# Optimization experiments

Hardware: AMD Instinct MI355X
Metric: run time of the kernel (lower is better)

The kernel has to match this reference:

```python
import jax, jax.numpy as jnp
import numpy as np

B, T, CIN, HID, OUT, H, W = 8, 8, 128, 64, 64, 32, 32


def _conv(x, w, b):
    # x: [B, C, H, W], w: [O, C, kh, kw] -> SAME-padded conv, stride 1
    y = jax.lax.conv_general_dilated(x, w, (1, 1), "SAME",
                                     dimension_numbers=("NCHW", "OIHW", "NCHW"))
    return y + b[None, :, None, None]


def _layer_dir(xs, w_ih, w_hh, b_ih, b_hh, reverse):
    # xs: [T, B, C, H, W]; one direction of a ConvLSTM layer; returns hs [T, B, HID, H, W]
    b, hh_, ww_ = xs.shape[1], xs.shape[3], xs.shape[4]
    h0 = jnp.zeros((b, HID, hh_, ww_), xs.dtype)

    def step(carry, x):
        h, c = carry
        gates = _conv(x, w_ih, b_ih) + _conv(h, w_hh, b_hh)  # [B, 4*HID, H, W]
        i, f, g, o = jnp.split(gates, 4, axis=1)
        c = jax.nn.sigmoid(f) * c + jax.nn.sigmoid(i) * jnp.tanh(g)
        h = jax.nn.sigmoid(o) * jnp.tanh(c)
        return (h, c), h

    _, hs = jax.lax.scan(step, (h0, h0), xs, reverse=reverse)
    return hs


def _forward(features, w_ih0f, w_hh0f, b_ih0f, b_hh0f,
             w_ih0r, w_hh0r, b_ih0r, b_hh0r,
             w_ih1f, w_hh1f, b_ih1f, b_hh1f,
             w_ih1r, w_hh1r, b_ih1r, b_hh1r,
             w_out, b_out):
    xs = jnp.transpose(features, (1, 0, 2, 3, 4))  # [T, B, C, H, W]
    # layer 0, both directions (scan reverse=True aligns outputs to original time order)
    hf = _layer_dir(xs, w_ih0f, w_hh0f, b_ih0f, b_hh0f, False)
    hr = _layer_dir(xs, w_ih0r, w_hh0r, b_ih0r, b_hh0r, True)
    xs1 = jnp.concatenate([hf, hr], axis=2)  # [T, B, 2*HID, H, W] (dropout is identity at eval)
    # layer 1
    hf1 = _layer_dir(xs1, w_ih1f, w_hh1f, b_ih1f, b_hh1f, False)
    hr1 = _layer_dir(xs1, w_ih1r, w_hh1r, b_ih1r, b_hh1r, True)
    last = jnp.concatenate([hf1[-1], hr1[-1]], axis=1)  # output[:, -1] -> [B, 2*HID, H, W]
    return jax.nn.relu(_conv(last, w_out, b_out))


def setup_inputs() -> dict:
    key = jax.random.key(0)
    ks = jax.random.split(key, 24)
    G = 4 * HID
    p = lambda k, s: jax.random.normal(k, s, jnp.float32) * 0.05
    d = {"features": jax.random.normal(ks[0], (B, T, CIN, H, W), jnp.float32)}
    i = 1
    for l, cin in ((0, CIN), (1, 2 * HID)):
        for dr in ("f", "r"):
            d[f"w_ih{l}{dr}"] = p(ks[i], (G, cin, 3, 3)); i += 1
            d[f"w_hh{l}{dr}"] = p(ks[i], (G, HID, 3, 3)); i += 1
            d[f"b_ih{l}{dr}"] = p(ks[i], (G,)); i += 1
            d[f"b_hh{l}{dr}"] = p(ks[i], (G,)); i += 1
    d["w_out"] = p(ks[i], (OUT, 2 * HID, 1, 1)); i += 1
    d["b_out"] = p(ks[i], (OUT,))
    return d


def reference(features, w_ih0f, w_hh0f, b_ih0f, b_hh0f,
              w_ih0r, w_hh0r, b_ih0r, b_hh0r,
              w_ih1f, w_hh1f, b_ih1f, b_hh1f,
              w_ih1r, w_hh1r, b_ih1r, b_hh1r,
              w_out, b_out):
    return _forward(features, w_ih0f, w_hh0f, b_ih0f, b_hh0f,
                    w_ih0r, w_hh0r, b_ih0r, b_hh0r,
                    w_ih1f, w_hh1f, b_ih1f, b_hh1f,
                    w_ih1r, w_hh1r, b_ih1r, b_hh1r,
                    w_out, b_out)
```

## Files before the change

### kernel.cpp

```cpp
#include <hip/hip_runtime.h>
#include <math.h>
#include <stdint.h>


typedef __attribute__((ext_vector_type(8))) short short8;
typedef __attribute__((ext_vector_type(4))) float float4v;

namespace {
constexpr int IMG = 34 * 34 * 64;
constexpr size_t SLOTI = 16ull * IMG;
constexpr int ROWB = 34 * 128;
constexpr int PADB = 8192;
}
template <int N> struct IC { static constexpr int v = N; };

__device__ __forceinline__ uint16_t bf16_rne(float x) {
  uint32_t u = __builtin_bit_cast(uint32_t, x);
  return (uint16_t)((u + 0x7FFFu + ((u >> 16) & 1u)) >> 16);
}
__device__ __forceinline__ float bf16_to_f(uint16_t h) {
  uint32_t u = ((uint32_t)h) << 16;
  return __builtin_bit_cast(float, u);
}

__device__ __forceinline__ void gl_lds16(const void* g, void* l) {
  __builtin_amdgcn_global_load_lds(
      (const __attribute__((address_space(1))) void*)g,
      (__attribute__((address_space(3))) void*)l, 16, 0, 0);
}

__global__ void pack_features(const float* __restrict__ f, uint16_t* __restrict__ out) {
  const size_t i = (size_t)blockIdx.x * 256 + threadIdx.x;
  const int blk_s = (int)(i & 7);
  size_t pp = i >> 3;
  const int px = (int)(pp % 34); pp /= 34;
  const int yy = (int)(pp % 34); pp /= 34;
  const int cg = (int)(pp & 3);
  const int bt = (int)(pp >> 2);
  const int b = bt & 7, t = bt >> 3;
  const int blk = blk_s ^ (px & 7);
  const int pl = blk >> 2, kg = blk & 3;
  short8 sv;
  if (px == 0 || px == 33 || yy == 0 || yy == 33) {
    #pragma unroll
    for (int j = 0; j < 8; ++j) sv[j] = 0;
  } else {
    const int x = px - 1, y = yy - 1;
    #pragma unroll
    for (int j = 0; j < 8; ++j) {
      const int ch = cg * 32 + kg * 8 + j;
      const float fv = f[(((size_t)b * 8 + t) * 128 + ch) * 1024 + y * 32 + x];
      const uint16_t hi = bf16_rne(fv);
      sv[j] = (short)(pl ? bf16_rne(fv - bf16_to_f(hi)) : hi);
    }
  }
  *(short8*)(out + i * 8) = sv;
}

struct WPackArgs {
  const float* wih[4]; const float* whh[4];
  const float* bih[4]; const float* bhh[4];
  uint32_t* wp; float* bp;
};
__global__ void pack_weights(WPackArgs A) {
  const int combo = blockIdx.y;
  const int idx = blockIdx.x * 256 + threadIdx.x;
  const int q = idx & 4095;
  const int rest = idx >> 12;
  const int nt = rest & 1;
  const int ct = rest >> 1;
  const int tap = ct % 9, cg = ct / 9;
  const int w2 = q & 3;
  const int b8s = (q >> 2) & 7;
  const int hcp = (q >> 5) & 15;
  const int g = (q >> 9) & 3;
  const int pl = (q >> 11) & 1;
  const int b8 = b8s ^ (hcp & 7);
  const int kg = b8 & 3;
  const int hcl = hcp * 2 + (b8 >> 2);
  const int n = g * 64 + nt * 32 + hcl;
  const float* wih = A.wih[combo];
  const float* whh = A.whh[combo];
  uint32_t out = 0;
  #pragma unroll
  for (int e = 0; e < 2; ++e) {
    const int ch = cg * 32 + kg * 8 + w2 * 2 + e;
    const float wv = (ch < 128) ? wih[((size_t)n * 128 + ch) * 9 + tap]
                                : whh[((size_t)n * 64 + (ch - 128)) * 9 + tap];
    const uint16_t hi = bf16_rne(wv);
    const uint16_t v = pl ? bf16_rne(wv - bf16_to_f(hi)) : hi;
    out |= ((uint32_t)v) << (16 * e);
  }
  A.wp[(size_t)combo * 442368 + idx] = out;
  if (idx < 256) A.bp[combo * 256 + idx] = A.bih[combo][idx] + A.bhh[combo][idx];
}

struct StepArgs {
  const uint16_t* in0; const uint16_t* in1; const uint16_t* in2;
  int nc0, nc1, nc2;
  const uint32_t* W;
  const float* bias;
  float* cbuf;
  uint16_t* himg;
  float* hf32;
};

struct Frags { short8 a[2][2]; short8 w[2][4]; };

__global__ __launch_bounds__(512, 2) void conv_lstm_step(StepArgs A0, StepArgs A1) {
  extern __shared__ char smem[];
  char* Asm_ = smem;
  char* Wsm_ = smem + 65536;

  const StepArgs a = (blockIdx.z == 0) ? A0 : A1;
  const int bx = blockIdx.x;
  const int nt = bx & 1;
  const int band = (bx >> 1) & 7;
  const int b = bx >> 4;
  const int y0 = band * 4;
  const int tid = threadIdx.x;
  const int lane = tid & 63;
  const int w = tid >> 6;
  const int m15 = lane & 15;
  const int kg = lane >> 4;
  const int r = w & 3;
  const int hcg = w >> 2;

  int offA[2][3][2];
  #pragma unroll
  for (int xh = 0; xh < 2; ++xh)
    #pragma unroll
    for (int kx = 0; kx < 3; ++kx)
      #pragma unroll
      for (int pl = 0; pl < 2; ++pl) {
        const int px = xh * 16 + kx + m15;
        const int sw = (pl * 4 + kg) ^ (px & 7);
        offA[xh][kx][pl] = r * ROWB + px * 128 + sw * 16;
      }
  int offW[2][4];
  {
    const int hcp = hcg * 8 + (m15 >> 1);
    const int b8 = kg + 4 * (m15 & 1);
    #pragma unroll
    for (int pl = 0; pl < 2; ++pl)
      #pragma unroll
      for (int g = 0; g < 4; ++g)
        offW[pl][g] = (((pl * 4 + g) * 16 + hcp) * 8 + (b8 ^ (hcp & 7))) * 16;
  }

  const int ncg = a.nc0 + a.nc1 + a.nc2;
  auto abase = [&](int cg) -> const char* {
    const uint16_t* t;
    if (cg < a.nc0) t = a.in0 + ((size_t)b * a.nc0 + cg) * IMG;
    else if (cg < a.nc0 + a.nc1) t = a.in1 + ((size_t)b * a.nc1 + (cg - a.nc0)) * IMG;
    else t = a.in2 + ((size_t)b * a.nc2 + (cg - a.nc0 - a.nc1)) * IMG;
    return (const char*)t + (size_t)y0 * ROWB;
  };
  auto stageA = [&](int cgi, int par) {
    const char* g = abase(cgi);
    char* d = Asm_ + par * 32768;
    #pragma unroll
    for (int j = 0; j < 4; ++j)
      gl_lds16(g + (size_t)(4 * w + j) * 1024 + lane * 16, d + (4 * w + j) * 1024);
  };
  auto stageW = [&](int cgs, int taps, int slot) {
    const char* g = (const char*)a.W + ((size_t)((cgs * 9 + taps) * 2 + nt) << 14);
    char* d = Wsm_ + slot * 16384;
    #pragma unroll
    for (int j = 0; j < 2; ++j)
      gl_lds16(g + (size_t)(2 * w + j) * 1024 + lane * 16, d + (2 * w + j) * 1024);
  };
  auto read_frags = [&](auto tapc, int cgn, int lin1) -> Frags {
    constexpr int TN = decltype(tapc)::v;
    constexpr int ky = TN / 3, kx = TN % 3;
    Frags f;
    const char* Ab = Asm_ + (cgn & 1) * 32768 + ky * ROWB;
    const char* Wb = Wsm_ + (lin1 & 3) * 16384;
    #pragma unroll
    for (int xh = 0; xh < 2; ++xh)
      #pragma unroll
      for (int pl = 0; pl < 2; ++pl)
        f.a[xh][pl] = *(const short8*)(Ab + offA[xh][kx][pl]);
    #pragma unroll
    for (int pl = 0; pl < 2; ++pl)
      #pragma unroll
      for (int g = 0; g < 4; ++g)
        f.w[pl][g] = *(const short8*)(Wb + offW[pl][g]);
    return f;
  };

  float4v acc[2][4];
  #pragma unroll
  for (int xh = 0; xh < 2; ++xh)
    #pragma unroll
    for (int g = 0; g < 4; ++g) acc[xh][g] = (float4v){0.f, 0.f, 0.f, 0.f};

  stageA(0, 0);
  stageW(0, 0, 0);
  stageW(0, 1, 1);
  stageW(0, 2, 2);
  asm volatile("s_waitcnt vmcnt(2)\n\ts_barrier" ::: "memory");
  Frags cur = read_frags(IC<0>{}, 0, 0);

  for (int cg = 0; cg < ncg; ++cg) {
    auto tap_body = [&](auto tapc) {
      constexpr int TAP = decltype(tapc)::v;
      constexpr int CNT = (TAP == 1 || TAP == 2) ? 6 : 2;
      asm volatile("s_waitcnt vmcnt(%0)\n\ts_barrier" :: "n"(CNT) : "memory");
      const int lin = cg * 9 + TAP;
      {
        const int l3 = lin + 3;
        int cgs = l3 / 9;
        const int taps = l3 % 9;
        if (cgs >= ncg) cgs = 0;
        stageW(cgs, taps, l3 & 3);
      }
      if (TAP == 0) {
        const int nx = (cg + 1 < ncg) ? cg + 1 : 0;
        stageA(nx, (cg + 1) & 1);
      }
      constexpr int TN = (TAP + 1) % 9;
      Frags nxt = read_frags(IC<TN>{}, cg + (TAP == 8 ? 1 : 0), lin + 1);
      #pragma unroll
      for (int xh = 0; xh < 2; ++xh)
        #pragma unroll
        for (int g = 0; g < 4; ++g) {
          acc[xh][g] = __builtin_amdgcn_mfma_f32_16x16x32_bf16(cur.a[xh][0], cur.w[0][g], acc[xh][g], 0, 0, 0);
          acc[xh][g] = __builtin_amdgcn_mfma_f32_16x16x32_bf16(cur.a[xh][0], cur.w[1][g], acc[xh][g], 0, 0, 0);
          acc[xh][g] = __builtin_amdgcn_mfma_f32_16x16x32_bf16(cur.a[xh][1], cur.w[0][g], acc[xh][g], 0, 0, 0);
        }
      cur = nxt;
    };
    tap_body(IC<0>{}); tap_body(IC<1>{}); tap_body(IC<2>{});
    tap_body(IC<3>{}); tap_body(IC<4>{}); tap_body(IC<5>{});
    tap_body(IC<6>{}); tap_body(IC<7>{}); tap_body(IC<8>{});
  }
  asm volatile("s_waitcnt vmcnt(0)" ::: "memory");

  const int hcl = hcg * 16 + m15;
  const int hc = nt * 32 + hcl;
  const int y = y0 + r;
  float bi[4];
  #pragma unroll
  for (int g = 0; g < 4; ++g) bi[g] = a.bias[g * 64 + hc];
  float* crow = a.cbuf + ((size_t)(b * 64 + hc)) * 1024 + y * 32;
  float* hrow = a.hf32 ? a.hf32 + ((size_t)(b * 64 + hc)) * 1024 + y * 32 : nullptr;
  uint16_t* hb = a.himg ? a.himg + ((size_t)(b * 2 + nt)) * IMG : nullptr;
  const int kgb = hcl >> 3, jj = hcl & 7;
  #pragma unroll
  for (int xh = 0; xh < 2; ++xh) {
    const int x0 = xh * 16 + kg * 4;
    float4v cv = *(float4v*)(crow + x0);
    float4v cn, hn;
    #pragma unroll
    for (int q = 0; q < 4; ++q) {
      const float ig = 1.f / (1.f + expf(-(acc[xh][0][q] + bi[0])));
      const float fg = 1.f / (1.f + expf(-(acc[xh][1][q] + bi[1])));
      const float gg = tanhf(acc[xh][2][q] + bi[2]);
      const float og = 1.f / (1.f + expf(-(acc[xh][3][q] + bi[3])));
      const float c2 = fg * cv[q] + ig * gg;
      cn[q] = c2;
      hn[q] = og * tanhf(c2);
    }
    *(float4v*)(crow + x0) = cn;
    if (hrow) *(float4v*)(hrow + x0) = hn;
    if (hb) {
      #pragma unroll
      for (int q = 0; q < 4; ++q) {
        const int px = x0 + q + 1;
        const int sw = px & 7;
        const uint16_t hi = bf16_rne(hn[q]);
        const uint16_t lo = bf16_rne(hn[q] - bf16_to_f(hi));
        const size_t p16 = ((size_t)(y + 1) * 34 + px) * 64;
        hb[p16 + (size_t)(kgb ^ sw) * 8 + jj] = hi;
        hb[p16 + (size_t)((4 + kgb) ^ sw) * 8 + jj] = lo;
      }
    }
  }
  if (hb) {
    {
      const int rr = tid >> 7;
      const int hlf = (tid >> 6) & 1;
      const int jx = tid & 63;
      hb[((size_t)(y0 + 1 + rr) * 34 + hlf * 33) * 64 + jx] = 0;
    }
    if (band == 0) for (int i = tid; i < 2176; i += 512) hb[i] = 0;
    if (band == 7) for (int i = tid; i < 2176; i += 512) hb[(size_t)33 * 2176 + i] = 0;
  }
}

__global__ void final_conv(const float* __restrict__ h1f_last, const float* __restrict__ h1r_last,
                           const float* __restrict__ wout, const float* __restrict__ bout,
                           float* __restrict__ out) {
  __shared__ float Ws[16 * 128];
  const int oq = blockIdx.y;
  for (int i = threadIdx.x; i < 16 * 128; i += 256) Ws[i] = wout[oq * 16 * 128 + i];
  __syncthreads();
  const int gp = blockIdx.x * 256 + threadIdx.x;
  const int b = gp >> 10, p = gp & 1023;
  float acc[16];
  #pragma unroll
  for (int o = 0; o < 16; ++o) acc[o] = bout[oq * 16 + o];
  for (int c = 0; c < 128; ++c) {
    const float xv = (c < 64) ? h1f_last[((size_t)b * 64 + c) * 1024 + p]
                              : h1r_last[((size_t)b * 64 + (c - 64)) * 1024 + p];
    #pragma unroll
    for (int o = 0; o < 16; ++o) acc[o] = fmaf(xv, Ws[o * 128 + c], acc[o]);
  }
  #pragma unroll
  for (int o = 0; o < 16; ++o) {
    const float v = acc[o];
    out[((size_t)b * 64 + oq * 16 + o) * 1024 + p] = v > 0.f ? v : 0.f;
  }
}

extern "C" void kernel_launch(void* const* d_in, const int* in_sizes, int n_in,
                              void* d_out, int out_size, void* d_ws, size_t ws_size,
                              hipStream_t stream) {
  char* p = (char*)d_ws;
  uint16_t* featImg = (uint16_t*)p; p += (size_t)8 * 8 * 4 * IMG * 2 + PADB;
  uint32_t* WP = (uint32_t*)p;      p += (size_t)4 * 442368 * 4;
  float* bp = (float*)p;            p += 4096;
  uint16_t* hf0i = (uint16_t*)p;    p += (size_t)9 * SLOTI * 2 + PADB;
  uint16_t* hr0i = (uint16_t*)p;    p += (size_t)9 * SLOTI * 2 + PADB;
  uint16_t* h1fi = (uint16_t*)p;    p += (size_t)2 * SLOTI * 2 + PADB;
  float* c0f = (float*)p;           p += (size_t)4 * 2097152;
  float* c0r = c0f + 524288;
  float* c1f = c0r + 524288;
  float* c1r = c1f + 524288;
  float* h1f8 = (float*)p;          p += 2097152;
  float* h1r8 = (float*)p;          p += 2097152;

  hipMemsetAsync(c0f, 0, (size_t)4 * 2097152, stream);
  hipMemsetAsync(hf0i, 0, (size_t)SLOTI * 2, stream);
  hipMemsetAsync(hr0i + (size_t)8 * SLOTI, 0, (size_t)SLOTI * 2, stream);
  hipMemsetAsync(h1fi, 0, (size_t)SLOTI * 2, stream);

  pack_features<<<dim3(9248), 256, 0, stream>>>((const float*)d_in[0], featImg);

  WPackArgs wa;
  for (int combo = 0; combo < 4; ++combo) {
    const int base = 1 + combo * 4;
    wa.wih[combo] = (const float*)d_in[base];
    wa.whh[combo] = (const float*)d_in[base + 1];
    wa.bih[combo] = (const float*)d_in[base + 2];
    wa.bhh[combo] = (const float*)d_in[base + 3];
  }
  wa.wp = WP; wa.bp = bp;
  pack_weights<<<dim3(1728, 4), 256, 0, stream>>>(wa);

  constexpr int DYN_LDS = 131072;
  (void)hipFuncSetAttribute((const void*)conv_lstm_step,
                            hipFuncAttributeMaxDynamicSharedMemorySize, DYN_LDS);

  auto mk = [&](const uint16_t* i0, int n0, const uint16_t* i1, int n1,
                const uint16_t* i2, int n2, int combo, float* cb,
                uint16_t* himg, float* hf32) {
    StepArgs s;
    s.in0 = i0; s.in1 = i1; s.in2 = i2;
    s.nc0 = n0; s.nc1 = n1; s.nc2 = n2;
    s.W = WP + (size_t)combo * 442368; s.bias = bp + combo * 256;
    s.cbuf = cb; s.himg = himg; s.hf32 = hf32;
    return s;
  };

  for (int k = 0; k < 8; ++k) {
    const int tr = 7 - k;
    StepArgs f = mk(featImg + (size_t)k * 8 * 4 * IMG, 4,
                    hf0i + (size_t)k * SLOTI, 2, nullptr, 0,
                    0, c0f, hf0i + (size_t)(k + 1) * SLOTI, nullptr);
    StepArgs r = mk(featImg + (size_t)tr * 8 * 4 * IMG, 4,
                    hr0i + (size_t)(tr + 1) * SLOTI, 2, nullptr, 0,
                    1, c0r, hr0i + (size_t)tr * SLOTI, nullptr);
    conv_lstm_step<<<dim3(128, 1, 2), 512, DYN_LDS, stream>>>(f, r);
  }

  for (int t = 0; t < 8; ++t) {
    uint16_t* himg = (t < 7) ? h1fi + (size_t)((t + 1) & 1) * SLOTI : nullptr;
    float* hf32 = (t == 7) ? h1f8 : nullptr;
    StepArgs s = mk(hf0i + (size_t)(t + 1) * SLOTI, 2, hr0i + (size_t)t * SLOTI, 2,
                    h1fi + (size_t)(t & 1) * SLOTI, 2, 2, c1f, himg, hf32);
    if (t == 0) {
      StepArgs rv = mk(hf0i + (size_t)8 * SLOTI, 2, hr0i + (size_t)7 * SLOTI, 2,
                       nullptr, 0, 3, c1r, nullptr, h1r8);
      conv_lstm_step<<<dim3(128, 1, 2), 512, DYN_LDS, stream>>>(s, rv);
    } else {
      conv_lstm_step<<<dim3(128, 1, 1), 512, DYN_LDS, stream>>>(s, s);
    }
  }

  final_conv<<<dim3(32, 4), 256, 0, stream>>>(
      h1f8, h1r8, (const float*)d_in[17], (const float*)d_in[18], (float*)d_out);
}
```

Measured before the change: 773.9 us.

## Halve workgroup size, raise per-wave M tile, add band-size templated launches

The ConvLSTM step kernel now runs 4 waves per workgroup instead of 8. Each wave owns multiple rows of M fragments (MROWS/2 rows x 2 halves), so each weight fragment read from LDS feeds more MFMAs. The kernel is templated on rows per band: layer 0 keeps 4-row bands with 128 blocks, and layer 1 uses 2-row bands with 256 blocks to fill more CUs in the sequential steps. It also double-buffers fragments explicitly with asm register pinning and changes the staging chunk counts and waitcnt thresholds to match. The risks are higher register pressure, lower occupancy (launch bounds 256,1) and fragile vmcnt accounting.

After: 750.0 us. 1.03x faster.

```diff
diff --git a/kernel.cpp b/kernel.cpp
--- a/kernel.cpp
+++ b/kernel.cpp
@@ -27,6 +27,22 @@
   __builtin_amdgcn_global_load_lds(
       (const __attribute__((address_space(1))) void*)g,
       (__attribute__((address_space(3))) void*)l, 16, 0, 0);
+}
+
+template <int NMF> struct Frags { short8 a[NMF][2]; short8 w[2][4]; };
+
+__device__ __forceinline__ void pin_frags(Frags<4>& f) {
+  asm volatile("" : "+v"(f.a[0][0]), "+v"(f.a[0][1]), "+v"(f.a[1][0]), "+v"(f.a[1][1]),
+                    "+v"(f.a[2][0]), "+v"(f.a[2][1]), "+v"(f.a[3][0]), "+v"(f.a[3][1]),
+                    "+v"(f.w[0][0]), "+v"(f.w[0][1]), "+v"(f.w[0][2]), "+v"(f.w[0][3]),
+                    "+v"(f.w[1][0]), "+v"(f.w[1][1]), "+v"(f.w[1][2]), "+v"(f.w[1][3])
+               :: "memory");
+}
+__device__ __forceinline__ void pin_frags(Frags<2>& f) {
+  asm volatile("" : "+v"(f.a[0][0]), "+v"(f.a[0][1]), "+v"(f.a[1][0]), "+v"(f.a[1][1]),
+                    "+v"(f.w[0][0]), "+v"(f.w[0][1]), "+v"(f.w[0][2]), "+v"(f.w[0][3]),
+                    "+v"(f.w[1][0]), "+v"(f.w[1][1]), "+v"(f.w[1][2]), "+v"(f.w[1][3])
+               :: "memory");
 }
 
 __global__ void pack_features(const float* __restrict__ f, uint16_t* __restrict__ out) {
@@ -105,9 +121,12 @@
   float* hf32;
 };
 
-struct Frags { short8 a[2][2]; short8 w[2][4]; };
-
-__global__ __launch_bounds__(512, 2) void conv_lstm_step(StepArgs A0, StepArgs A1) {
+template <int MROWS>
+__global__ __launch_bounds__(256, 1) void conv_lstm_step(StepArgs A0, StepArgs A1) {
+  constexpr int R = MROWS / 2;
+  constexpr int NMF = MROWS;
+  constexpr int ACH = (MROWS == 4) ? 7 : 5;
+  constexpr int NBANDS = 32 / MROWS;
   extern __shared__ char smem[];
   char* Asm_ = smem;
   char* Wsm_ = smem + 65536;
@@ -115,18 +134,18 @@
   const StepArgs a = (blockIdx.z == 0) ? A0 : A1;
   const int bx = blockIdx.x;
   const int nt = bx & 1;
-  const int band = (bx >> 1) & 7;
-  const int b = bx >> 4;
-  const int y0 = band * 4;
+  const int band = (bx >> 1) & (NBANDS - 1);
+  const int b = bx >> ((MROWS == 4) ? 4 : 5);
+  const int y0 = band * MROWS;
   const int tid = threadIdx.x;
   const int lane = tid & 63;
   const int w = tid >> 6;
   const int m15 = lane & 15;
   const int kg = lane >> 4;
-  const int r = w & 3;
-  const int hcg = w >> 2;
-
-  int offA[2][3][2];
+  const int hcg = w & 1;
+  const int mh = w >> 1;
+
+  int offA0[2][3][2];
   #pragma unroll
   for (int xh = 0; xh < 2; ++xh)
     #pragma unroll
@@ -135,7 +154,7 @@
       for (int pl = 0; pl < 2; ++pl) {
         const int px = xh * 16 + kx + m15;
         const int sw = (pl * 4 + kg) ^ (px & 7);
-        offA[xh][kx][pl] = r * ROWB + px * 128 + sw * 16;
+        offA0[xh][kx][pl] = px * 128 + sw * 16;
       }
   int offW[2][4];
   {
@@ -147,6 +166,7 @@
       for (int g = 0; g < 4; ++g)
         offW[pl][g] = (((pl * 4 + g) * 16 + hcp) * 8 + (b8 ^ (hcp & 7))) * 16;
   }
+  const int mrow = mh * R * ROWB;
 
   const int ncg = a.nc0 + a.nc1 + a.nc2;
   auto abase = [&](int cg) -> const char* {
@@ -160,132 +180,157 @@
     const char* g = abase(cgi);
     char* d = Asm_ + par * 32768;
     #pragma unroll
-    for (int j = 0; j < 4; ++j)
-      gl_lds16(g + (size_t)(4 * w + j) * 1024 + lane * 16, d + (4 * w + j) * 1024);
+    for (int j = 0; j < ACH; ++j)
+      gl_lds16(g + (size_t)(ACH * w + j) * 1024 + lane * 16, d + (ACH * w + j) * 1024);
   };
   auto stageW = [&](int cgs, int taps, int slot) {
     const char* g = (const char*)a.W + ((size_t)((cgs * 9 + taps) * 2 + nt) << 14);
     char* d = Wsm_ + slot * 16384;
     #pragma unroll
-    for (int j = 0; j < 2; ++j)
-      gl_lds16(g + (size_t)(2 * w + j) * 1024 + lane * 16, d + (2 * w + j) * 1024);
-  };
-  auto read_frags = [&](auto tapc, int cgn, int lin1) -> Frags {
-    constexpr int TN = decltype(tapc)::v;
+    for (int j = 0; j < 4; ++j)
+      gl_lds16(g + (size_t)(4 * w + j) * 1024 + lane * 16, d + (4 * w + j) * 1024);
+  };
+
+  Frags<NMF> f0, f1;
+  auto read_frags = [&](auto tnc, int par, int wslot, Frags<NMF>& f) {
+    constexpr int TN = decltype(tnc)::v;
     constexpr int ky = TN / 3, kx = TN % 3;
-    Frags f;
-    const char* Ab = Asm_ + (cgn & 1) * 32768 + ky * ROWB;
-    const char* Wb = Wsm_ + (lin1 & 3) * 16384;
-    #pragma unroll
-    for (int xh = 0; xh < 2; ++xh)
-      #pragma unroll
-      for (int pl = 0; pl < 2; ++pl)
-        f.a[xh][pl] = *(const short8*)(Ab + offA[xh][kx][pl]);
+    const char* Ab = Asm_ + par * 32768 + mrow;
+    const char* Wb = Wsm_ + wslot * 16384;
+    #pragma unroll
+    for (int rr = 0; rr < R; ++rr)
+      #pragma unroll
+      for (int xh = 0; xh < 2; ++xh)
+        #pragma unroll
+        for (int pl = 0; pl < 2; ++pl)
+          f.a[rr * 2 + xh][pl] = *(const short8*)(Ab + (rr + ky) * ROWB + offA0[xh][kx][pl]);
     #pragma unroll
     for (int pl = 0; pl < 2; ++pl)
       #pragma unroll
       for (int g = 0; g < 4; ++g)
         f.w[pl][g] = *(const short8*)(Wb + offW[pl][g]);
-    return f;
-  };
-
-  float4v acc[2][4];
-  #pragma unroll
-  for (int xh = 0; xh < 2; ++xh)
-    #pragma unroll
-    for (int g = 0; g < 4; ++g) acc[xh][g] = (float4v){0.f, 0.f, 0.f, 0.f};
+  };
+
+  float4v acc[NMF][4];
+  #pragma unroll
+  for (int mf = 0; mf < NMF; ++mf)
+    #pragma unroll
+    for (int g = 0; g < 4; ++g) acc[mf][g] = (float4v){0.f, 0.f, 0.f, 0.f};
+
+  auto do_mfma = [&](Frags<NMF>& f) {
+    #pragma unroll
+    for (int mf = 0; mf < NMF; ++mf)
+      #pragma unroll
+      for (int g = 0; g < 4; ++g) {
+        acc[mf][g] = __builtin_amdgcn_mfma_f32_16x16x32_bf16(f.a[mf][0], f.w[0][g], acc[mf][g], 0, 0, 0);
+        acc[mf][g] = __builtin_amdgcn_mfma_f32_16x16x32_bf16(f.a[mf][0], f.w[1][g], acc[mf][g], 0, 0, 0);
+        acc[mf][g] = __builtin_amdgcn_mfma_f32_16x16x32_bf16(f.a[mf][1], f.w[0][g], acc[mf][g], 0, 0, 0);
+      }
+  };
+
+  auto window = [&](auto tapc, auto parc, int cg, int lin9) {
+    constexpr int TAP = decltype(tapc)::v;
+    constexpr int P = decltype(parc)::v;
+    constexpr int CNT = (TAP == 1 || TAP == 2) ? 4 + ACH : 4;
+    asm volatile("s_waitcnt vmcnt(%0)\n\ts_barrier" :: "n"(CNT) : "memory");
+    {
+      const int l3 = lin9 + TAP + 3;
+      int cgs = l3 / 9;
+      const int taps = l3 % 9;
+      if (cgs >= ncg) cgs = 0;
+      stageW(cgs, taps, l3 & 3);
+    }
+    if (TAP == 0) {
+      const int nx = (cg + 1 < ncg) ? cg + 1 : 0;
+      stageA(nx, (cg + 1) & 1);
+    }
+    constexpr int TN = (TAP + 1) % 9;
+    const int cgn = cg + (TAP == 8 ? 1 : 0);
+    read_frags(IC<TN>{}, cgn & 1, (lin9 + TAP + 1) & 3, P ? f0 : f1);
+    Frags<NMF>& cur = P ? f1 : f0;
+    pin_frags(cur);
+    do_mfma(cur);
+  };
+  auto run9 = [&](auto cgpc, int cg) {
+    constexpr int CGP = decltype(cgpc)::v;
+    const int lin9 = cg * 9;
+    window(IC<0>{}, IC<(CGP + 0) & 1>{}, cg, lin9);
+    window(IC<1>{}, IC<(CGP + 1) & 1>{}, cg, lin9);
+    window(IC<2>{}, IC<(CGP + 2) & 1>{}, cg, lin9);
+    window(IC<3>{}, IC<(CGP + 3) & 1>{}, cg, lin9);
+    window(IC<4>{}, IC<(CGP + 4) & 1>{}, cg, lin9);
+    window(IC<5>{}, IC<(CGP + 5) & 1>{}, cg, lin9);
+    window(IC<6>{}, IC<(CGP + 6) & 1>{}, cg, lin9);
+    window(IC<7>{}, IC<(CGP + 7) & 1>{}, cg, lin9);
+    window(IC<8>{}, IC<(CGP + 8) & 1>{}, cg, lin9);
+  };
 
   stageA(0, 0);
   stageW(0, 0, 0);
   stageW(0, 1, 1);
   stageW(0, 2, 2);
-  asm volatile("s_waitcnt vmcnt(2)\n\ts_barrier" ::: "memory");
-  Frags cur = read_frags(IC<0>{}, 0, 0);
+  asm volatile("s_waitcnt vmcnt(8)\n\ts_barrier" ::: "memory");
+  read_frags(IC<0>{}, 0, 0, f0);
 
   for (int cg = 0; cg < ncg; ++cg) {
-    auto tap_body = [&](auto tapc) {
-      constexpr int TAP = decltype(tapc)::v;
-      constexpr int CNT = (TAP == 1 || TAP == 2) ? 6 : 2;
-      asm volatile("s_waitcnt vmcnt(%0)\n\ts_barrier" :: "n"(CNT) : "memory");
-      const int lin = cg * 9 + TAP;
-      {
-        const int l3 = lin + 3;
-        int cgs = l3 / 9;
-        const int taps = l3 % 9;
-        if (cgs >= ncg) cgs = 0;
-        stageW(cgs, taps, l3 & 3);
-      }
-      if (TAP == 0) {
-        const int nx = (cg + 1 < ncg) ? cg + 1 : 0;
-        stageA(nx, (cg + 1) & 1);
-      }
-      constexpr int TN = (TAP + 1) % 9;
-      Frags nxt = read_frags(IC<TN>{}, cg + (TAP == 8 ? 1 : 0), lin + 1);
-      #pragma unroll
-      for (int xh = 0; xh < 2; ++xh)
-        #pragma unroll
-        for (int g = 0; g < 4; ++g) {
-          acc[xh][g] = __builtin_amdgcn_mfma_f32_16x16x32_bf16(cur.a[xh][0], cur.w[0][g], acc[xh][g], 0, 0, 0);
-          acc[xh][g] = __builtin_amdgcn_mfma_f32_16x16x32_bf16(cur.a[xh][0], cur.w[1][g], acc[xh][g], 0, 0, 0);
-          acc[xh][g] = __builtin_amdgcn_mfma_f32_16x16x32_bf16(cur.a[xh][1], cur.w[0][g], acc[xh][g], 0, 0, 0);
-        }
-      cur = nxt;
-    };
-    tap_body(IC<0>{}); tap_body(IC<1>{}); tap_body(IC<2>{});
-    tap_body(IC<3>{}); tap_body(IC<4>{}); tap_body(IC<5>{});
-    tap_body(IC<6>{}); tap_body(IC<7>{}); tap_body(IC<8>{});
+    if ((cg & 1) == 0) run9(IC<0>{}, cg);
+    else run9(IC<1>{}, cg);
   }
   asm volatile("s_waitcnt vmcnt(0)" ::: "memory");
 
   const int hcl = hcg * 16 + m15;
   const int hc = nt * 32 + hcl;
-  const int y = y0 + r;
   float bi[4];
   #pragma unroll
   for (int g = 0; g < 4; ++g) bi[g] = a.bias[g * 64 + hc];
-  float* crow = a.cbuf + ((size_t)(b * 64 + hc)) * 1024 + y * 32;
-  float* hrow = a.hf32 ? a.hf32 + ((size_t)(b * 64 + hc)) * 1024 + y * 32 : nullptr;
   uint16_t* hb = a.himg ? a.himg + ((size_t)(b * 2 + nt)) * IMG : nullptr;
   const int kgb = hcl >> 3, jj = hcl & 7;
   #pragma unroll
-  for (int xh = 0; xh < 2; ++xh) {
-    const int x0 = xh * 16 + kg * 4;
-    float4v cv = *(float4v*)(crow + x0);
-    float4v cn, hn;
-    #pragma unroll
-    for (int q = 0; q < 4; ++q) {
-      const float ig = 1.f / (1.f + expf(-(acc[xh][0][q] + bi[0])));
-      const float fg = 1.f / (1.f + expf(-(acc[xh][1][q] + bi[1])));
-      const float gg = tanhf(acc[xh][2][q] + bi[2]);
-      const float og = 1.f / (1.f + expf(-(acc[xh][3][q] + bi[3])));
-      const float c2 = fg * cv[q] + ig * gg;
-      cn[q] = c2;
-      hn[q] = og * tanhf(c2);
-    }
-    *(float4v*)(crow + x0) = cn;
-    if (hrow) *(float4v*)(hrow + x0) = hn;
-    if (hb) {
+  for (int rr = 0; rr < R; ++rr) {
+    const int y = y0 + mh * R + rr;
+    float* crow = a.cbuf + ((size_t)(b * 64 + hc)) * 1024 + y * 32;
+    float* hrow = a.hf32 ? a.hf32 + ((size_t)(b * 64 + hc)) * 1024 + y * 32 : nullptr;
+    #pragma unroll
+    for (int xh = 0; xh < 2; ++xh) {
+      const int mf = rr * 2 + xh;
+      const int x0 = xh * 16 + kg * 4;
+      float4v cv = *(float4v*)(crow + x0);
+      float4v cn, hn;
       #pragma unroll
       for (int q = 0; q < 4; ++q) {
-        const int px = x0 + q + 1;
-        const int sw = px & 7;
-        const uint16_t hi = bf16_rne(hn[q]);
-        const uint16_t lo = bf16_rne(hn[q] - bf16_to_f(hi));
-        const size_t p16 = ((size_t)(y + 1) * 34 + px) * 64;
-        hb[p16 + (size_t)(kgb ^ sw) * 8 + jj] = hi;
-        hb[p16 + (size_t)((4 + kgb) ^ sw) * 8 + jj] = lo;
+        const float ig = 1.f / (1.f + expf(-(acc[mf][0][q] + bi[0])));
+        const float fg = 1.f / (1.f + expf(-(acc[mf][1][q] + bi[1])));
+        const float gg = tanhf(acc[mf][2][q] + bi[2]);
+        const float og = 1.f / (1.f + expf(-(acc[mf][3][q] + bi[3])));
+        const float c2 = fg * cv[q] + ig * gg;
+        cn[q] = c2;
+        hn[q] = og * tanhf(c2);
       }
+      *(float4v*)(crow + x0) = cn;
+      if (hrow) *(float4v*)(hrow + x0) = hn;
+      if (hb) {
+        #pragma unroll
+        for (int q = 0; q < 4; ++q) {
+          const int px = x0 + q + 1;
+          const int sw = px & 7;
+          const uint16_t hi = bf16_rne(hn[q]);
+          const uint16_t lo = bf16_rne(hn[q] - bf16_to_f(hi));
+          const size_t p16 = ((size_t)(y + 1) * 34 + px) * 64;
+          hb[p16 + (size_t)(kgb ^ sw) * 8 + jj] = hi;
+          hb[p16 + (size_t)((4 + kgb) ^ sw) * 8 + jj] = lo;
+        }
+      }
     }
   }
   if (hb) {
-    {
-      const int rr = tid >> 7;
-      const int hlf = (tid >> 6) & 1;
-      const int jx = tid & 63;
+    for (int i = tid; i < MROWS * 128; i += 256) {
+      const int rr = i >> 7;
+      const int hlf = (i >> 6) & 1;
+      const int jx = i & 63;
       hb[((size_t)(y0 + 1 + rr) * 34 + hlf * 33) * 64 + jx] = 0;
     }
-    if (band == 0) for (int i = tid; i < 2176; i += 512) hb[i] = 0;
-    if (band == 7) for (int i = tid; i < 2176; i += 512) hb[(size_t)33 * 2176 + i] = 0;
+    if (band == 0) for (int i = tid; i < 2176; i += 256) hb[i] = 0;
+    if (band == NBANDS - 1) for (int i = tid; i < 2176; i += 256) hb[(size_t)33 * 2176 + i] = 0;
   }
 }
 
@@ -350,7 +395,9 @@
   pack_weights<<<dim3(1728, 4), 256, 0, stream>>>(wa);
 
   constexpr int DYN_LDS = 131072;
-  (void)hipFuncSetAttribute((const void*)conv_lstm_step,
+  (void)hipFuncSetAttribute((const void*)conv_lstm_step<4>,
+                            hipFuncAttributeMaxDynamicSharedMemorySize, DYN_LDS);
+  (void)hipFuncSetAttribute((const void*)conv_lstm_step<2>,
                             hipFuncAttributeMaxDynamicSharedMemorySize, DYN_LDS);
 
   auto mk = [&](const uint16_t* i0, int n0, const uint16_t* i1, int n1,
@@ -372,7 +419,7 @@
     StepArgs r = mk(featImg + (size_t)tr * 8 * 4 * IMG, 4,
                     hr0i + (size_t)(tr + 1) * SLOTI, 2, nullptr, 0,
                     1, c0r, hr0i + (size_t)tr * SLOTI, nullptr);
-    conv_lstm_step<<<dim3(128, 1, 2), 512, DYN_LDS, stream>>>(f, r);
+    conv_lstm_step<4><<<dim3(128, 1, 2), 256, DYN_LDS, stream>>>(f, r);
   }
 
   for (int t = 0; t < 8; ++t) {
@@ -383,9 +430,9 @@
     if (t == 0) {
       StepArgs rv = mk(hf0i + (size_t)8 * SLOTI, 2, hr0i + (size_t)7 * SLOTI, 2,
                        nullptr, 0, 3, c1r, nullptr, h1r8);
-      conv_lstm_step<<<dim3(128, 1, 2), 512, DYN_LDS, stream>>>(s, rv);
+      conv_lstm_step<2><<<dim3(256, 1, 2), 256, DYN_LDS, stream>>>(s, rv);
     } else {
-      conv_lstm_step<<<dim3(128, 1, 1), 512, DYN_LDS, stream>>>(s, s);
+      conv_lstm_step<2><<<dim3(256, 1, 1), 256, DYN_LDS, stream>>>(s, s);
     }
   }
 
```
